# Kernel tuning notes

Hardware: AMD Instinct MI355X
Metric: run time of the kernel (lower is better)

## Reference

```python
import jax, jax.numpy as jnp
import numpy as np

N = 4096   # number of nodes
E = 4096   # number of hyperedges
F_IN = 128
F_OUT = 128
AVG_DEG = 32.0


def setup_inputs() -> dict:
    key = jax.random.key(0)
    k_x, k_h, k_w = jax.random.split(key, 3)
    X = jax.random.normal(k_x, (N, F_IN), dtype=jnp.float32)
    # Binary incidence matrix with average node degree ~AVG_DEG
    H = (jax.random.uniform(k_h, (N, E)) < (AVG_DEG / E)).astype(jnp.float32)
    # Diagonal degree matrices (clamped >= 1 so they are invertible)
    dv = jnp.maximum(H.sum(axis=1), 1.0)   # [N] vertex degrees
    de = jnp.maximum(H.sum(axis=0), 1.0)   # [E] hyperedge degrees
    D_v = jnp.diag(dv)                     # [N, N]
    D_e = jnp.diag(de)                     # [E, E]
    # Xavier-uniform weight
    limit = float(np.sqrt(6.0 / (F_IN + F_OUT)))
    W = jax.random.uniform(k_w, (F_IN, F_OUT), minval=-limit, maxval=limit,
                           dtype=jnp.float32)
    return {"X": X, "H": H, "D_v": D_v, "D_e": D_e, "W": W}


def reference(X, H, D_v, D_e, W):
    # Faithful to torch: generic matrix inverse of the (diagonal) degree matrices
    D_v_inv = jnp.linalg.inv(D_v)          # [N, N]
    D_e_inv = jnp.linalg.inv(D_e)          # [E, E]
    theta = X @ W                          # [N, F_out]
    coeff = D_v_inv @ H                    # [N, E]
    coeff = coeff @ D_e_inv                # [N, E]
    coeff = coeff @ H.T                    # [N, N]
    return coeff @ theta                   # [N, F_out]
```

## Files before the change

kernel.cpp:

```cpp
#include <hip/hip_runtime.h>

constexpr int N = 4096;
constexpr int E = 4096;
constexpr int F = 128;
constexpr int MAXL = 128;
constexpr int DIAG_LD = 4097;

__device__ __forceinline__ ushort f2bf_rne(float x) {
    union { float f; unsigned u; } v; v.f = x;
    return (ushort)((v.u + 0x7FFFu + ((v.u >> 16) & 1u)) >> 16);
}

__global__ __launch_bounds__(256) void k_fused1(
        const float* __restrict__ H,
        const float* __restrict__ X,
        const float* __restrict__ Wm,
        unsigned long long* __restrict__ BM,
        int* __restrict__ row_cnt,
        ushort* __restrict__ row_list,
        ushort* __restrict__ theta_bf) {
    __shared__ float smem[16 * F];
    const int t = threadIdx.x;

    if (blockIdx.x < (unsigned)N) {
        ushort* sL   = (ushort*)smem;
        int*    lcnt = (int*)(smem + 128);
        const int wave = t >> 6, lane = t & 63;
        if (t == 0) *lcnt = 0;
        __syncthreads();
        const int r = blockIdx.x;
        const float* Hr = H + (size_t)r * E;
        uint4 v[4];
        #pragma unroll
        for (int s = 0; s < 4; ++s)
            v[s] = *(const uint4*)&Hr[(wave * 256 + s * 64 + lane) * 4];
        unsigned long long wreg = 0;
        #pragma unroll
        for (int s = 0; s < 4; ++s) {
            const uint vv[4] = {v[s].x, v[s].y, v[s].z, v[s].w};
            #pragma unroll
            for (int c = 0; c < 4; ++c) {
                const unsigned long long m = __ballot(vv[c] != 0u);
                if (lane == s * 4 + c) wreg = m;
                if (vv[c]) {
                    const int p = atomicAdd(lcnt, 1);
                    if (p < MAXL)
                        sL[p] = (ushort)(wave * 1024 + s * 256 + 4 * lane + c);
                }
            }
        }
        if (lane < 16)
            BM[(size_t)r * 64 + wave * 16 + lane] = wreg;
        __syncthreads();
        if (wave == 0) {
            ((uint*)&row_list[(size_t)r * MAXL])[lane] = ((const uint*)sL)[lane];
            if (lane == 0) row_cnt[r] = *lcnt < MAXL ? *lcnt : MAXL;
        }
    } else {
        float (*Xs)[F] = (float(*)[F])smem;
        const int r0 = (blockIdx.x - N) * 16;
        #pragma unroll
        for (int i = 0; i < 2; ++i) {
            const int idx = i * 256 + t;
            const int rr = idx >> 5, cc = (idx & 31) * 4;
            *(float4*)&Xs[rr][cc] = *(const float4*)&X[(size_t)(r0 + rr) * F + cc];
        }
        __syncthreads();
        const int f = t & 127, half = t >> 7;
        float acc[8];
        #pragma unroll
        for (int i = 0; i < 8; ++i) acc[i] = 0.f;
        #pragma unroll 4
        for (int k = 0; k < F; ++k) {
            const float w = Wm[k * F + f];
            #pragma unroll
            for (int i = 0; i < 8; ++i) acc[i] += Xs[half * 8 + i][k] * w;
        }
        #pragma unroll
        for (int i = 0; i < 8; ++i)
            theta_bf[(size_t)(r0 + half * 8 + i) * F + f] = f2bf_rne(acc[i]);
    }
}

__global__ __launch_bounds__(512) void k_pass2(
        const unsigned long long* __restrict__ BM,
        int* __restrict__ col_cnt,
        ushort* __restrict__ col_list) {
    __shared__ ushort sL[64][MAXL];
    __shared__ int cnt[64];
    const int t = threadIdx.x, wave = t >> 6, lane = t & 63;
    const int wc = blockIdx.x;
    if (t < 64) cnt[t] = 0;
    __syncthreads();
    unsigned long long w8[8];
    #pragma unroll
    for (int j = 0; j < 8; ++j)
        w8[j] = BM[(size_t)(wave * 512 + j * 64 + lane) * 64 + wc];
    #pragma unroll
    for (int j = 0; j < 8; ++j) {
        unsigned long long m = w8[j];
        const ushort row = (ushort)(wave * 512 + j * 64 + lane);
        while (m) {
            const int b = __builtin_ctzll(m); m &= m - 1;
            const int p = atomicAdd(&cnt[b], 1);
            if (p < MAXL) sL[b][p] = row;
        }
    }
    __syncthreads();
    const int el = t >> 3, ch = t & 7;
    const int e = (wc >> 2) * 256 + 4 * el + (wc & 3);
    const uint4* src = (const uint4*)sL[el];
    uint4* dst = (uint4*)&col_list[(size_t)e * MAXL];
    dst[ch * 2 + 0] = src[ch * 2 + 0];
    dst[ch * 2 + 1] = src[ch * 2 + 1];
    if (ch == 0) col_cnt[e] = cnt[el] < MAXL ? cnt[el] : MAXL;
}

template <bool OUT_BF16>
__global__ __launch_bounds__(256) void k_spmm(const int* __restrict__ cnt,
                                              const ushort* __restrict__ list,
                                              const ushort* __restrict__ Vin,
                                              const float* __restrict__ Dmat,
                                              void* __restrict__ Vout) {
    __shared__ ushort sIdx[4][MAXL];
    const int t = threadIdx.x, wave = t >> 6, lane = t & 63;
    const int r = blockIdx.x * 4 + wave;
    *(ushort2*)&sIdx[wave][lane * 2] =
        *(const ushort2*)&list[(size_t)r * MAXL + lane * 2];
    int c = cnt[r]; c = c < MAXL ? c : MAXL;
    const float dscale = 1.0f / Dmat[(size_t)r * DIAG_LD];
    __syncthreads();
    const char* vb = (const char*)Vin;
    float a0 = 0.f, a1 = 0.f;
    int i = 0;
    for (; i + 16 <= c; i += 16) {
        uint v[16];
        #pragma unroll
        for (int j = 0; j < 16; ++j)
            v[j] = *(const uint*)(vb + ((int)sIdx[wave][i + j] * 256 + lane * 4));
        #pragma unroll
        for (int j = 0; j < 16; ++j) {
            a0 += __uint_as_float((v[j] & 0xffffu) << 16);
            a1 += __uint_as_float((v[j] >> 16) << 16);
        }
    }
    for (; i + 4 <= c; i += 4) {
        uint v[4];
        #pragma unroll
        for (int j = 0; j < 4; ++j)
            v[j] = *(const uint*)(vb + ((int)sIdx[wave][i + j] * 256 + lane * 4));
        #pragma unroll
        for (int j = 0; j < 4; ++j) {
            a0 += __uint_as_float((v[j] & 0xffffu) << 16);
            a1 += __uint_as_float((v[j] >> 16) << 16);
        }
    }
    for (; i < c; ++i) {
        const uint v = *(const uint*)(vb + ((int)sIdx[wave][i] * 256 + lane * 4));
        a0 += __uint_as_float((v & 0xffffu) << 16);
        a1 += __uint_as_float((v >> 16) << 16);
    }
    a0 *= dscale; a1 *= dscale;
    if (OUT_BF16) {
        ushort2 o; o.x = f2bf_rne(a0); o.y = f2bf_rne(a1);
        *(ushort2*)((ushort*)Vout + (size_t)r * F + lane * 2) = o;
    } else {
        float2 o; o.x = a0; o.y = a1;
        *(float2*)((float*)Vout + (size_t)r * F + lane * 2) = o;
    }
}

extern "C" void kernel_launch(void* const* d_in, const int* in_sizes, int n_in,
                              void* d_out, int out_size, void* d_ws, size_t ws_size,
                              hipStream_t stream) {
    const float* X  = (const float*)d_in[0];
    const float* H  = (const float*)d_in[1];
    const float* Dv = (const float*)d_in[2];
    const float* De = (const float*)d_in[3];
    const float* W  = (const float*)d_in[4];
    float* out = (float*)d_out;
    char* ws = (char*)d_ws;

    ushort* theta    = (ushort*)ws;
    unsigned long long* BM =
        (unsigned long long*)(ws + (size_t)1 * 1024 * 1024);
    ushort* M        = (ushort*)(ws + (size_t)1 * 1024 * 1024);
    ushort* row_list = (ushort*)(ws + (size_t)3 * 1024 * 1024);
    ushort* col_list = (ushort*)(ws + (size_t)4 * 1024 * 1024);
    int*    row_cnt  = (int*)   (ws + (size_t)5 * 1024 * 1024);
    int*    col_cnt  = row_cnt + N;

    k_fused1<<<dim3(N + N / 16), dim3(256), 0, stream>>>(
        H, X, W, BM, row_cnt, row_list, theta);
    k_pass2<<<dim3(64), dim3(512), 0, stream>>>(BM, col_cnt, col_list);
    k_spmm<true ><<<dim3(E / 4), dim3(256), 0, stream>>>(col_cnt, col_list,
                                                         theta, De, M);
    k_spmm<false><<<dim3(N / 4), dim3(256), 0, stream>>>(row_cnt, row_list,
                                                         M, Dv, out);
}
```

Before: 199.4 us.

## Fuse column-list build into edge SpMM, dropping col_list round trip

Merges the transpose/column-list construction kernel with the hyperedge aggregation SpMM. Each block builds 64 edge lists in shared memory and immediately gathers theta rows to produce the bf16 edge features. This removes a kernel launch and the global write/read of col_list and col_cnt. The trade-off is that the edge aggregation now runs on only 64 large blocks, which reduces parallelism and latency hiding for the gather.

```diff
diff --git a/kernel.cpp b/kernel.cpp
--- a/kernel.cpp
+++ b/kernel.cpp
@@ -82,24 +82,25 @@
     }
 }
 
-__global__ __launch_bounds__(512) void k_pass2(
+__global__ __launch_bounds__(1024) void k_edge(
         const unsigned long long* __restrict__ BM,
-        int* __restrict__ col_cnt,
-        ushort* __restrict__ col_list) {
+        const ushort* __restrict__ theta,
+        const float* __restrict__ De,
+        ushort* __restrict__ M) {
     __shared__ ushort sL[64][MAXL];
     __shared__ int cnt[64];
     const int t = threadIdx.x, wave = t >> 6, lane = t & 63;
     const int wc = blockIdx.x;
     if (t < 64) cnt[t] = 0;
     __syncthreads();
-    unsigned long long w8[8];
+    unsigned long long w4[4];
     #pragma unroll
-    for (int j = 0; j < 8; ++j)
-        w8[j] = BM[(size_t)(wave * 512 + j * 64 + lane) * 64 + wc];
+    for (int j = 0; j < 4; ++j)
+        w4[j] = BM[(size_t)(wave * 256 + j * 64 + lane) * 64 + wc];
     #pragma unroll
-    for (int j = 0; j < 8; ++j) {
-        unsigned long long m = w8[j];
-        const ushort row = (ushort)(wave * 512 + j * 64 + lane);
+    for (int j = 0; j < 4; ++j) {
+        unsigned long long m = w4[j];
+        const ushort row = (ushort)(wave * 256 + j * 64 + lane);
         while (m) {
             const int b = __builtin_ctzll(m); m &= m - 1;
             const int p = atomicAdd(&cnt[b], 1);
@@ -107,21 +108,52 @@
         }
     }
     __syncthreads();
-    const int el = t >> 3, ch = t & 7;
-    const int e = (wc >> 2) * 256 + 4 * el + (wc & 3);
-    const uint4* src = (const uint4*)sL[el];
-    uint4* dst = (uint4*)&col_list[(size_t)e * MAXL];
-    dst[ch * 2 + 0] = src[ch * 2 + 0];
-    dst[ch * 2 + 1] = src[ch * 2 + 1];
-    if (ch == 0) col_cnt[e] = cnt[el] < MAXL ? cnt[el] : MAXL;
-}
-
-template <bool OUT_BF16>
-__global__ __launch_bounds__(256) void k_spmm(const int* __restrict__ cnt,
-                                              const ushort* __restrict__ list,
-                                              const ushort* __restrict__ Vin,
-                                              const float* __restrict__ Dmat,
-                                              void* __restrict__ Vout) {
+    const char* vb = (const char*)theta;
+    #pragma unroll
+    for (int i4 = 0; i4 < 4; ++i4) {
+        const int el = wave * 4 + i4;
+        const int e  = (wc >> 2) * 256 + 4 * el + (wc & 3);
+        int c = cnt[el]; c = c < MAXL ? c : MAXL;
+        const float dscale = 1.0f / De[(size_t)e * DIAG_LD];
+        float a0 = 0.f, a1 = 0.f;
+        int i = 0;
+        for (; i + 16 <= c; i += 16) {
+            uint v[16];
+            #pragma unroll
+            for (int j = 0; j < 16; ++j)
+                v[j] = *(const uint*)(vb + ((int)sL[el][i + j] * 256 + lane * 4));
+            #pragma unroll
+            for (int j = 0; j < 16; ++j) {
+                a0 += __uint_as_float((v[j] & 0xffffu) << 16);
+                a1 += __uint_as_float((v[j] >> 16) << 16);
+            }
+        }
+        for (; i + 4 <= c; i += 4) {
+            uint v[4];
+            #pragma unroll
+            for (int j = 0; j < 4; ++j)
+                v[j] = *(const uint*)(vb + ((int)sL[el][i + j] * 256 + lane * 4));
+            #pragma unroll
+            for (int j = 0; j < 4; ++j) {
+                a0 += __uint_as_float((v[j] & 0xffffu) << 16);
+                a1 += __uint_as_float((v[j] >> 16) << 16);
+            }
+        }
+        for (; i < c; ++i) {
+            const uint v = *(const uint*)(vb + ((int)sL[el][i] * 256 + lane * 4));
+            a0 += __uint_as_float((v & 0xffffu) << 16);
+            a1 += __uint_as_float((v >> 16) << 16);
+        }
+        ushort2 o; o.x = f2bf_rne(a0 * dscale); o.y = f2bf_rne(a1 * dscale);
+        *(ushort2*)&M[(size_t)e * F + lane * 2] = o;
+    }
+}
+
+__global__ __launch_bounds__(256) void k_spmm2(const int* __restrict__ cnt,
+                                               const ushort* __restrict__ list,
+                                               const ushort* __restrict__ Vin,
+                                               const float* __restrict__ Dmat,
+                                               float* __restrict__ Vout) {
     __shared__ ushort sIdx[4][MAXL];
     const int t = threadIdx.x, wave = t >> 6, lane = t & 63;
     const int r = blockIdx.x * 4 + wave;
@@ -160,14 +192,8 @@
         a0 += __uint_as_float((v & 0xffffu) << 16);
         a1 += __uint_as_float((v >> 16) << 16);
     }
-    a0 *= dscale; a1 *= dscale;
-    if (OUT_BF16) {
-        ushort2 o; o.x = f2bf_rne(a0); o.y = f2bf_rne(a1);
-        *(ushort2*)((ushort*)Vout + (size_t)r * F + lane * 2) = o;
-    } else {
-        float2 o; o.x = a0; o.y = a1;
-        *(float2*)((float*)Vout + (size_t)r * F + lane * 2) = o;
-    }
+    float2 o; o.x = a0 * dscale; o.y = a1 * dscale;
+    *(float2*)&Vout[(size_t)r * F + lane * 2] = o;
 }
 
 extern "C" void kernel_launch(void* const* d_in, const int* in_sizes, int n_in,
@@ -184,17 +210,12 @@
     ushort* theta    = (ushort*)ws;
     unsigned long long* BM =
         (unsigned long long*)(ws + (size_t)1 * 1024 * 1024);
-    ushort* M        = (ushort*)(ws + (size_t)1 * 1024 * 1024);
     ushort* row_list = (ushort*)(ws + (size_t)3 * 1024 * 1024);
-    ushort* col_list = (ushort*)(ws + (size_t)4 * 1024 * 1024);
+    ushort* M        = (ushort*)(ws + (size_t)4 * 1024 * 1024);
     int*    row_cnt  = (int*)   (ws + (size_t)5 * 1024 * 1024);
-    int*    col_cnt  = row_cnt + N;
 
     k_fused1<<<dim3(N + N / 16), dim3(256), 0, stream>>>(
         H, X, W, BM, row_cnt, row_list, theta);
-    k_pass2<<<dim3(64), dim3(512), 0, stream>>>(BM, col_cnt, col_list);
-    k_spmm<true ><<<dim3(E / 4), dim3(256), 0, stream>>>(col_cnt, col_list,
-                                                         theta, De, M);
-    k_spmm<false><<<dim3(N / 4), dim3(256), 0, stream>>>(row_cnt, row_list,
-                                                         M, Dv, out);
-}
+    k_edge<<<dim3(64), dim3(1024), 0, stream>>>(BM, theta, De, M);
+    k_spmm2<<<dim3(N / 4), dim3(256), 0, stream>>>(row_cnt, row_list, M, Dv, out);
+}
```

Result: no change. 201.9 us (+1.3%).
